# Performance work log

Measured on AMD Instinct MI355X. Metric: run time of the kernel, lower is better.

Reference implementation:

```python
import jax, jax.numpy as jnp
import numpy as np

D_MODEL = 256
D_STATE = 64
D_CONV = 4
EXPAND = 2
HEADDIM = 16
D_INNER = EXPAND * D_MODEL            # 512
NHEADS = D_INNER // HEADDIM           # 32
CONV_DIM = D_INNER + 2 * D_STATE      # 640 (ngroups=1)
D_IN_PROJ = 2 * D_INNER + 2 * D_STATE + NHEADS  # 1184
BATCH = 256
SEQ = 200


def _ln(x, g, b, eps=1e-12):
    m = jnp.mean(x, axis=-1, keepdims=True)
    v = jnp.mean((x - m) ** 2, axis=-1, keepdims=True)
    return (x - m) * jax.lax.rsqrt(v + eps) * g + b


def setup_inputs() -> dict:
    key = jax.random.key(0)
    ks = jax.random.split(key, 16)
    def gn(i, shape, s=0.02):
        return jax.random.normal(ks[i], shape, jnp.float32) * s
    return {
        "input_tensor": jax.random.normal(ks[0], (BATCH, SEQ, D_MODEL), jnp.float32),
        # Mamba2 params
        "in_proj_w": gn(1, (D_MODEL, D_IN_PROJ)),
        "conv_w": gn(2, (CONV_DIM, D_CONV), 0.1),
        "conv_b": jnp.zeros((CONV_DIM,), jnp.float32),
        "dt_bias": gn(3, (NHEADS,), 0.1),
        "A_log": jnp.log(jax.random.uniform(ks[4], (NHEADS,), jnp.float32, 1.0, 16.0)),
        "D_skip": jnp.ones((NHEADS,), jnp.float32),
        "rms_w": jnp.ones((D_INNER,), jnp.float32),
        "out_proj_w": gn(5, (D_INNER, D_MODEL)),
        # Layer norms / mixers
        "ln_g": jnp.ones((D_MODEL,), jnp.float32),
        "ln_b": jnp.zeros((D_MODEL,), jnp.float32),
        "filt_w": gn(6, (1, SEQ // 2 + 1, D_MODEL, 2), 0.02),
        "filt_ln_g": jnp.ones((D_MODEL,), jnp.float32),
        "filt_ln_b": jnp.zeros((D_MODEL,), jnp.float32),
        "alpha": jax.random.uniform(ks[7], (D_MODEL,), jnp.float32),
        "beta": jax.random.uniform(ks[8], (D_MODEL,), jnp.float32),
        # FFN
        "ffn_w1": gn(9, (D_MODEL, 4 * D_MODEL)),
        "ffn_b1": jnp.zeros((4 * D_MODEL,), jnp.float32),
        "ffn_w2": gn(10, (4 * D_MODEL, D_MODEL)),
        "ffn_b2": jnp.zeros((D_MODEL,), jnp.float32),
        "ffn_ln_g": jnp.ones((D_MODEL,), jnp.float32),
        "ffn_ln_b": jnp.zeros((D_MODEL,), jnp.float32),
    }


def _mamba2(x, in_proj_w, conv_w, conv_b, dt_bias, A_log, D_skip, rms_w, out_proj_w):
    b, l, _ = x.shape
    zxbcdt = x @ in_proj_w                                  # [b,l,1184]
    z, xBC, dt = jnp.split(zxbcdt, [D_INNER, D_INNER + CONV_DIM], axis=-1)
    # depthwise causal conv over time + SiLU
    xp = jnp.pad(xBC, ((0, 0), (D_CONV - 1, 0), (0, 0)))
    conv = conv_b + sum(conv_w[:, k] * xp[:, k:k + l, :] for k in range(D_CONV))
    xBC = jax.nn.silu(conv)
    xs, Bm, Cm = jnp.split(xBC, [D_INNER, D_INNER + D_STATE], axis=-1)
    xh = xs.reshape(b, l, NHEADS, HEADDIM)
    dt = jax.nn.softplus(dt + dt_bias)                      # [b,l,h]
    A = -jnp.exp(A_log)                                     # [h]
    dA = jnp.exp(dt * A)                                    # [b,l,h]
    dtx = dt[..., None] * xh                                # [b,l,h,p]

    def step(state, inp):
        dA_t, dtx_t, B_t, C_t = inp
        # state: [b,h,p,n]
        state = dA_t[:, :, None, None] * state + dtx_t[..., None] * B_t[:, None, None, :]
        y_t = jnp.einsum('bhpn,bn->bhp', state, C_t)
        return state, y_t

    state0 = jnp.zeros((b, NHEADS, HEADDIM, D_STATE), x.dtype)
    _, y = jax.lax.scan(step, state0,
                        (jnp.moveaxis(dA, 1, 0), jnp.moveaxis(dtx, 1, 0),
                         jnp.moveaxis(Bm, 1, 0), jnp.moveaxis(Cm, 1, 0)))
    y = jnp.moveaxis(y, 0, 1) + D_skip[None, None, :, None] * xh   # skip connection
    y = y.reshape(b, l, D_INNER)
    # gated RMSNorm: rmsnorm(y * silu(z)) * w
    g = y * jax.nn.silu(z)
    g = g * jax.lax.rsqrt(jnp.mean(g * g, axis=-1, keepdims=True) + 1e-5) * rms_w
    return g @ out_proj_w


def reference(input_tensor, in_proj_w, conv_w, conv_b, dt_bias, A_log, D_skip,
              rms_w, out_proj_w, ln_g, ln_b, filt_w, filt_ln_g, filt_ln_b,
              alpha, beta, ffn_w1, ffn_b1, ffn_w2, ffn_b2, ffn_ln_g, ffn_ln_b):
    x = input_tensor
    h1 = _mamba2(x, in_proj_w, conv_w, conv_b, dt_bias, A_log, D_skip, rms_w, out_proj_w)
    h1 = _ln(h1 + x, ln_g, ln_b)
    # FFT filter branch
    xf = jnp.fft.rfft(x, axis=1, norm='ortho')
    w = filt_w[..., 0] + 1j * filt_w[..., 1]                # [1,101,d]
    xi = jnp.fft.irfft(xf * w, n=SEQ, axis=1, norm='ortho').astype(x.dtype)
    h2 = _ln(xi + x, filt_ln_g, filt_ln_b)
    h = alpha * h1 + beta * h2
    hid = jax.nn.gelu(h @ ffn_w1 + ffn_b1, approximate=False) @ ffn_w2 + ffn_b2
    return _ln(hid + h, ffn_ln_g, ffn_ln_b)
```

## Files before the change

kernel.cpp:

```cpp
#include <hip/hip_runtime.h>
#include <math.h>

#define BATCHN 256
#define SEQ 200
#define DMODEL 256
#define DINNER 512
#define NH 32
#define HD 16
#define DSTATE 64
#define DINPROJ 1184
#define XBCLD 672
#define BL (BATCHN*SEQ)
#define NF 101
#define NJ 202
#define XBASE 655360
#define TC 20
#define NCH 10
#define XIOFF 8500000

typedef __attribute__((ext_vector_type(8))) short bf16x8;
typedef __attribute__((ext_vector_type(4))) float f32x4;

__device__ inline unsigned short f2bf(float f) {
    union { float f; unsigned u; } v; v.f = f;
    unsigned r = v.u + 0x7FFFu + ((v.u >> 16) & 1u);
    return (unsigned short)(r >> 16);
}
__device__ inline float bf2f(unsigned short h) {
    union { unsigned u; float f; } v; v.u = ((unsigned)h) << 16;
    return v.f;
}

#define GLOAD16(src, dst) __builtin_amdgcn_global_load_lds( \
    (const __attribute__((address_space(1))) void*)(src),   \
    (__attribute__((address_space(3))) void*)(dst), 16, 0, 0)

__global__ void init_dft_kernel(unsigned short* __restrict__ EF, unsigned short* __restrict__ EI)
{
    const float ang = 6.28318530717958647692f / 200.0f;
    int idx = blockIdx.x * 256 + threadIdx.x;
    if (idx < 256 * SEQ) {
        int f = idx / SEQ, t = idx - f * SEQ;
        float v;
        if (f <= 100) { int ph = (f * t) % 200; v = cosf(ang * (float)ph); }
        else if (f <= 201) { int ff = f - 101; int ph = (ff * t) % 200; v = -sinf(ang * (float)ph); }
        else v = 0.f;
        EF[idx] = f2bf(v);
    } else if (idx < 256 * SEQ + 256 * 256) {
        int j2 = idx - 256 * SEQ;
        int t = j2 >> 8, j = j2 & 255;
        float v;
        if (t >= 200) v = 0.f;
        else if (j == 0) v = 1.0f / 200.0f;
        else if (j == 100) v = ((t & 1) ? -1.0f : 1.0f) / 200.0f;
        else if (j < 100) { int ph = (j * t) % 200; v = 2.0f * cosf(ang * (float)ph) / 200.0f; }
        else if (j >= 202 || j == 101 || j == 201) v = 0.0f;
        else { int f = j - 101; int ph = (f * t) % 200; v = -2.0f * sinf(ang * (float)ph) / 200.0f; }
        EI[j2] = f2bf(v);
    }
}

__global__ void pack_wT_kernel(const float* __restrict__ src, unsigned short* __restrict__ dst,
                               int srcld, int coloff, int N, int K)
{
    int idx = blockIdx.x * 256 + threadIdx.x;
    if (idx >= N * K) return;
    int n = idx / K, k = idx - n * K;
    dst[idx] = f2bf(src[(long long)k * srcld + coloff + n]);
}

__global__ void f2bf_kernel(const float* __restrict__ X, unsigned short* __restrict__ O)
{
    long long i = ((long long)blockIdx.x * 256 + threadIdx.x) * 8;
    float4 a = ((const float4*)(X + i))[0];
    float4 b = ((const float4*)(X + i))[1];
    uint4 o;
    o.x = (unsigned)f2bf(a.x) | ((unsigned)f2bf(a.y) << 16);
    o.y = (unsigned)f2bf(a.z) | ((unsigned)f2bf(a.w) << 16);
    o.z = (unsigned)f2bf(b.x) | ((unsigned)f2bf(b.y) << 16);
    o.w = (unsigned)f2bf(b.z) | ((unsigned)f2bf(b.w) << 16);
    *(uint4*)(O + i) = o;
}

__global__ void xT_kernel(const float* __restrict__ X, unsigned short* __restrict__ XT)
{
    __shared__ float tile[32][33];
    int b = blockIdx.z, t0 = blockIdx.x * 32, d0 = blockIdx.y * 32;
    int tx = threadIdx.x & 31, ty = threadIdx.x >> 5;
    const float* xb = X + (long long)b * SEQ * DMODEL;
#pragma unroll
    for (int i = 0; i < 4; i++) {
        int t = t0 + ty + i * 8;
        tile[ty + i * 8][tx] = (t < SEQ) ? xb[(long long)t * DMODEL + d0 + tx] : 0.f;
    }
    __syncthreads();
    unsigned short* xtb = XT + (long long)b * DMODEL * SEQ;
#pragma unroll
    for (int i = 0; i < 4; i++) {
        int d = d0 + ty + i * 8;
        int t = t0 + tx;
        if (t < SEQ) xtb[(long long)d * SEQ + t] = f2bf(tile[tx][ty + i * 8]);
    }
}

template<int ACT, int CBF>
__global__ __launch_bounds__(256) void mgemm_kernel(
    const unsigned short* __restrict__ Ab, const unsigned short* __restrict__ BTp,
    void* __restrict__ Cp, const float* __restrict__ bias,
    int M, int N, int K, int lda, int ldbt, int ldc,
    long long sA, long long sBT, long long sC)
{
    __shared__ unsigned short As[128 * 32];
    __shared__ unsigned short Bs[128 * 32];
    const unsigned short* Aa = Ab + (long long)blockIdx.z * sA;
    const unsigned short* Bt = BTp + (long long)blockIdx.z * sBT;
    float* Cf = (float*)Cp + (CBF ? 0 : (long long)blockIdx.z * sC);
    unsigned short* Cb = (unsigned short*)Cp + (CBF ? (long long)blockIdx.z * sC : 0);

    int m0 = blockIdx.y * 128, n0 = blockIdx.x * 128;
    int tid = threadIdx.x;
    int srow = tid >> 1, skb = (tid & 1) * 16;
    int w = tid >> 6, l = tid & 63;
    int wr = w >> 1, wc = w & 1;
    int fr = l & 15, fk = l >> 4;
    int glr = (w << 4) + (l >> 2);
    int glc = (l & 3) << 3;
    bool fullM = (m0 + 128 <= M);
    bool fullN = (n0 + 128 <= N);

    f32x4 acc[4][4] = {};

    for (int k0 = 0; k0 < K; k0 += 32) {
        bool kedge = (k0 + 32 > K);
        if (fullM && !kedge) {
            GLOAD16(Aa + (long long)(m0 + glr) * lda + k0 + glc,      &As[w << 9]);
            GLOAD16(Aa + (long long)(m0 + 64 + glr) * lda + k0 + glc, &As[2048 + (w << 9)]);
        } else {
            int gm = m0 + srow;
            unsigned short* dst = &As[srow * 32 + skb];
#pragma unroll
            for (int i = 0; i < 16; i++) {
                int gk = k0 + skb + i;
                dst[i] = (gm < M && gk < K) ? Aa[(long long)gm * lda + gk] : (unsigned short)0;
            }
        }
        if (fullN && !kedge) {
            GLOAD16(Bt + (long long)(n0 + glr) * ldbt + k0 + glc,      &Bs[w << 9]);
            GLOAD16(Bt + (long long)(n0 + 64 + glr) * ldbt + k0 + glc, &Bs[2048 + (w << 9)]);
        } else {
            int gn = n0 + srow;
            unsigned short* dst = &Bs[srow * 32 + skb];
#pragma unroll
            for (int i = 0; i < 16; i++) {
                int gk = k0 + skb + i;
                dst[i] = (gn < N && gk < K) ? Bt[(long long)gn * ldbt + gk] : (unsigned short)0;
            }
        }
        __syncthreads();
        bf16x8 a[4], b[4];
#pragma unroll
        for (int i = 0; i < 4; i++) {
            a[i] = *(const bf16x8*)&As[(wr * 64 + i * 16 + fr) * 32 + fk * 8];
            b[i] = *(const bf16x8*)&Bs[(wc * 64 + i * 16 + fr) * 32 + fk * 8];
        }
#pragma unroll
        for (int i = 0; i < 4; i++)
#pragma unroll
            for (int j = 0; j < 4; j++)
                acc[i][j] = __builtin_amdgcn_mfma_f32_16x16x32_bf16(a[i], b[j], acc[i][j], 0, 0, 0);
        __syncthreads();
    }

#pragma unroll
    for (int i = 0; i < 4; i++) {
        int gr0 = m0 + wr * 64 + i * 16 + fk * 4;
#pragma unroll
        for (int j = 0; j < 4; j++) {
            int gc = n0 + wc * 64 + j * 16 + fr;
            if (gc >= N) continue;
            float bv = bias ? bias[gc] : 0.f;
#pragma unroll
            for (int r = 0; r < 4; r++) {
                int gr = gr0 + r;
                if (gr >= M) continue;
                float v = acc[i][j][r] + bv;
                if (ACT == 1) v = 0.5f * v * (1.f + erff(v * 0.70710678118654752f));
                long long ci = (long long)gr * ldc + gc;
                if (CBF) Cb[ci] = f2bf(v);
                else Cf[ci] = v;
            }
        }
    }
}

__global__ void convbc_kernel(const float* __restrict__ XBC, const float* __restrict__ conv_w,
                              const float* __restrict__ conv_b, const float* __restrict__ dt_bias,
                              const float* __restrict__ A_log,
                              float* __restrict__ BCb, float* __restrict__ DTb, float* __restrict__ DAb)
{
    int row = blockIdx.x;
    int b = row / SEQ, l = row - b * SEQ;
    int tid = threadIdx.x;
    if (tid < 128) {
        int ch = 512 + tid;
        float acc = conv_b[ch];
#pragma unroll
        for (int k = 0; k < 4; k++) {
            int lt = l + k - 3;
            if (lt >= 0)
                acc = fmaf(conv_w[ch * 4 + k], XBC[(long long)(b * SEQ + lt) * XBCLD + ch], acc);
        }
        BCb[(long long)row * 128 + tid] = acc * __builtin_amdgcn_rcpf(1.f + __expf(-acc));
    } else if (tid < 160) {
        int h = tid - 128;
        float draw = XBC[(long long)row * XBCLD + 640 + h] + dt_bias[h];
        float dtv = (draw > 20.f) ? draw : log1pf(__expf(draw));
        DTb[(long long)row * NH + h] = dtv;
        DAb[(long long)row * NH + h] = __expf(-__expf(A_log[h]) * dtv);
    }
}

__device__ __forceinline__ void sstep(
    float raw, float dtv, float da,
    const float4& qb0, const float4& qb1, const float4& qb2, const float4& qb3,
    const float4& qc0, const float4& qc1, const float4& qc2, const float4& qc3,
    float cw0, float cw1, float cw2, float cw3, float cb, float ds,
    float* st, float& w0, float& w1, float& w2,
    int lane, float* __restrict__ yaddr)
{
    float cvv = cb + cw0 * w0 + cw1 * w1 + cw2 * w2 + cw3 * raw;
    float xhv = cvv * __builtin_amdgcn_rcpf(1.f + __expf(-cvv));
    w0 = w1; w1 = w2; w2 = raw;
    float xv = dtv * xhv;
    float p0, p1, p2, p3;
    st[0]  = fmaf(da, st[0],  xv * qb0.x); p0 = st[0]  * qc0.x;
    st[1]  = fmaf(da, st[1],  xv * qb0.y); p1 = st[1]  * qc0.y;
    st[2]  = fmaf(da, st[2],  xv * qb0.z); p2 = st[2]  * qc0.z;
    st[3]  = fmaf(da, st[3],  xv * qb0.w); p3 = st[3]  * qc0.w;
    st[4]  = fmaf(da, st[4],  xv * qb1.x); p0 = fmaf(st[4],  qc1.x, p0);
    st[5]  = fmaf(da, st[5],  xv * qb1.y); p1 = fmaf(st[5],  qc1.y, p1);
    st[6]  = fmaf(da, st[6],  xv * qb1.z); p2 = fmaf(st[6],  qc1.z, p2);
    st[7]  = fmaf(da, st[7],  xv * qb1.w); p3 = fmaf(st[7],  qc1.w, p3);
    st[8]  = fmaf(da, st[8],  xv * qb2.x); p0 = fmaf(st[8],  qc2.x, p0);
    st[9]  = fmaf(da, st[9],  xv * qb2.y); p1 = fmaf(st[9],  qc2.y, p1);
    st[10] = fmaf(da, st[10], xv * qb2.z); p2 = fmaf(st[10], qc2.z, p2);
    st[11] = fmaf(da, st[11], xv * qb2.w); p3 = fmaf(st[11], qc2.w, p3);
    st[12] = fmaf(da, st[12], xv * qb3.x); p0 = fmaf(st[12], qc3.x, p0);
    st[13] = fmaf(da, st[13], xv * qb3.y); p1 = fmaf(st[13], qc3.y, p1);
    st[14] = fmaf(da, st[14], xv * qb3.z); p2 = fmaf(st[14], qc3.z, p2);
    st[15] = fmaf(da, st[15], xv * qb3.w); p3 = fmaf(st[15], qc3.w, p3);
    float part = (p0 + p1) + (p2 + p3);
    part += __shfl_xor(part, 16);
    part += __shfl_xor(part, 32);
    if (lane < HD) *yaddr = part + ds * xhv;
}

__global__ __launch_bounds__(256) void scan7_kernel(
    const float* __restrict__ DTb, const float* __restrict__ DAb,
    float* __restrict__ XBC, const float* __restrict__ BCb,
    const float* __restrict__ Dsk,
    const float* __restrict__ conv_w, const float* __restrict__ conv_b)
{
    __shared__ float sbc[2][TC][128];
    __shared__ unsigned short sx[2][TC][128];
    __shared__ float sdt[2][TC][8];
    __shared__ float sda[2][TC][8];
    int tid = threadIdx.x;
    int wv = tid >> 6, lane = tid & 63;
    int bid = blockIdx.x;
    int b = bid >> 2, hq = (bid & 3) * 8;
    long long rowb = (long long)b * SEQ;

    for (int i = tid; i < TC * 32; i += 256) {
        int r = i >> 5, c = i & 31;
        ((float4*)&sbc[0][r][0])[c] = ((const float4*)(BCb + (rowb + r) * 128))[c];
    }
    for (int i = tid; i < TC * 64; i += 256) {
        int r = i >> 6, c2 = i & 63;
        float2 v = *(const float2*)(XBC + (rowb + r) * XBCLD + hq * 16 + (c2 << 1));
        *(unsigned*)&sx[0][r][c2 << 1] = (unsigned)f2bf(v.x) | ((unsigned)f2bf(v.y) << 16);
    }
    for (int i = tid; i < TC * 8; i += 256) {
        int t = i >> 3, j = i & 7;
        sdt[0][t][j] = DTb[(rowb + t) * NH + hq + j];
        sda[0][t][j] = DAb[(rowb + t) * NH + hq + j];
    }
    __syncthreads();

    int p = lane & 15, g = lane >> 4;
    int hA = hq + wv, hB = hq + 4 + wv;
    int chA = hA * HD + p, chB = hB * HD + p;
    float cwA0 = conv_w[chA * 4 + 0], cwA1 = conv_w[chA * 4 + 1];
    float cwA2 = conv_w[chA * 4 + 2], cwA3 = conv_w[chA * 4 + 3];
    float cbA = conv_b[chA];
    float cwB0 = conv_w[chB * 4 + 0], cwB1 = conv_w[chB * 4 + 1];
    float cwB2 = conv_w[chB * 4 + 2], cwB3 = conv_w[chB * 4 + 3];
    float cbB = conv_b[chB];
    float dsA = Dsk[hA], dsB = Dsk[hB];
    int xcA = wv * 16 + p, xcB = (4 + wv) * 16 + p;
    float* ypA = XBC + rowb * XBCLD + hA * HD + p;
    float* ypB = XBC + rowb * XBCLD + hB * HD + p;
    float stA[16], stB[16];
#pragma unroll
    for (int r = 0; r < 16; r++) { stA[r] = 0.f; stB[r] = 0.f; }
    float wA0 = 0.f, wA1 = 0.f, wA2 = 0.f;
    float wB0 = 0.f, wB1 = 0.f, wB2 = 0.f;

    for (int c = 0; c < NCH; c++) {
        int cur = c & 1;
        if (c + 1 < NCH) {
            int nb = cur ^ 1;
            long long tb = rowb + (c + 1) * TC;
            for (int i = tid; i < TC * 32; i += 256) {
                int r = i >> 5, cc = i & 31;
                ((float4*)&sbc[nb][r][0])[cc] = ((const float4*)(BCb + (tb + r) * 128))[cc];
            }
            for (int i = tid; i < TC * 64; i += 256) {
                int r = i >> 6, c2 = i & 63;
                float2 v = *(const float2*)(XBC + (tb + r) * XBCLD + hq * 16 + (c2 << 1));
                *(unsigned*)&sx[nb][r][c2 << 1] = (unsigned)f2bf(v.x) | ((unsigned)f2bf(v.y) << 16);
            }
            for (int i = tid; i < TC * 8; i += 256) {
                int t = i >> 3, j = i & 7;
                sdt[nb][t][j] = DTb[(tb + t) * NH + hq + j];
                sda[nb][t][j] = DAb[(tb + t) * NH + hq + j];
            }
        }
        int tbase = c * TC;
        for (int t = 0; t < TC; t++) {
            int gt = tbase + t;
            const float4* qb = (const float4*)&sbc[cur][t][g * 16];
            const float4* qc = (const float4*)&sbc[cur][t][64 + g * 16];
            float4 qb0 = qb[0], qb1 = qb[1], qb2 = qb[2], qb3 = qb[3];
            float4 qc0 = qc[0], qc1 = qc[1], qc2 = qc[2], qc3 = qc[3];
            float rawA = bf2f(sx[cur][t][xcA]);
            float rawB = bf2f(sx[cur][t][xcB]);
            sstep(rawA, sdt[cur][t][wv], sda[cur][t][wv], qb0, qb1, qb2, qb3, qc0, qc1, qc2, qc3,
                  cwA0, cwA1, cwA2, cwA3, cbA, dsA, stA, wA0, wA1, wA2,
                  lane, ypA + (long long)gt * XBCLD);
            sstep(rawB, sdt[cur][t][4 + wv], sda[cur][t][4 + wv], qb0, qb1, qb2, qb3, qc0, qc1, qc2, qc3,
                  cwB0, cwB1, cwB2, cwB3, cbB, dsB, stB, wB0, wB1, wB2,
                  lane, ypB + (long long)gt * XBCLD);
        }
        __syncthreads();
    }
}

__global__ __launch_bounds__(256) void gate_kernel(
    float* __restrict__ XBC, const unsigned short* __restrict__ Zbf,
    const float* __restrict__ rms_w)
{
    int row = blockIdx.x * 4 + (threadIdx.x >> 6);
    int lane = threadIdx.x & 63;
    float* yrow = XBC + (long long)row * XBCLD + lane * 8;
    const unsigned short* zrow = Zbf + (long long)row * 512 + lane * 8;
    float4 y0 = ((const float4*)yrow)[0];
    float4 y1 = ((const float4*)yrow)[1];
    uint4 zq = ((const uint4*)zrow)[0];
    float yv[8] = { y0.x, y0.y, y0.z, y0.w, y1.x, y1.y, y1.z, y1.w };
    float zv[8];
    zv[0] = bf2f((unsigned short)(zq.x & 0xFFFF)); zv[1] = bf2f((unsigned short)(zq.x >> 16));
    zv[2] = bf2f((unsigned short)(zq.y & 0xFFFF)); zv[3] = bf2f((unsigned short)(zq.y >> 16));
    zv[4] = bf2f((unsigned short)(zq.z & 0xFFFF)); zv[5] = bf2f((unsigned short)(zq.z >> 16));
    zv[6] = bf2f((unsigned short)(zq.w & 0xFFFF)); zv[7] = bf2f((unsigned short)(zq.w >> 16));
    float a[8]; float ss = 0.f;
#pragma unroll
    for (int i = 0; i < 8; i++) {
        float z = zv[i];
        a[i] = yv[i] * (z * __builtin_amdgcn_rcpf(1.f + __expf(-z)));
        ss = fmaf(a[i], a[i], ss);
    }
#pragma unroll
    for (int m = 1; m < 64; m <<= 1) ss += __shfl_xor(ss, m);
    float sc = rsqrtf(ss * (1.f / 512.f) + 1e-5f);
    const float* rw = rms_w + lane * 8;
    float4 r0 = ((const float4*)rw)[0];
    float4 r1 = ((const float4*)rw)[1];
    float rv[8] = { r0.x, r0.y, r0.z, r0.w, r1.x, r1.y, r1.z, r1.w };
    uint4 o;
    o.x = (unsigned)f2bf(a[0] * sc * rv[0]) | ((unsigned)f2bf(a[1] * sc * rv[1]) << 16);
    o.y = (unsigned)f2bf(a[2] * sc * rv[2]) | ((unsigned)f2bf(a[3] * sc * rv[3]) << 16);
    o.z = (unsigned)f2bf(a[4] * sc * rv[4]) | ((unsigned)f2bf(a[5] * sc * rv[5]) << 16);
    o.w = (unsigned)f2bf(a[6] * sc * rv[6]) | ((unsigned)f2bf(a[7] * sc * rv[7]) << 16);
    unsigned short* grow = (unsigned short*)(XBC + (long long)row * XBCLD);
    ((uint4*)grow)[lane] = o;
}

__global__ void lnadd_bf_kernel(const unsigned short* __restrict__ A, const float* __restrict__ Bb,
                                const float* __restrict__ g, const float* __restrict__ be,
                                float* __restrict__ O)
{
    int row = blockIdx.x * 4 + (threadIdx.x >> 6);
    int lane = threadIdx.x & 63;
    long long base = (long long)row * DMODEL + lane * 4;
    float v[4]; float s1 = 0.f;
#pragma unroll
    for (int i = 0; i < 4; i++) { float a = bf2f(A[base + i]) + Bb[base + i]; v[i] = a; s1 += a; }
#pragma unroll
    for (int m = 1; m < 64; m <<= 1) s1 += __shfl_xor(s1, m);
    float mean = s1 * (1.f / 256.f);
    float s2 = 0.f;
#pragma unroll
    for (int i = 0; i < 4; i++) { float d = v[i] - mean; s2 = fmaf(d, d, s2); }
#pragma unroll
    for (int m = 1; m < 64; m <<= 1) s2 += __shfl_xor(s2, m);
    float r = rsqrtf(s2 * (1.f / 256.f) + 1e-12f);
#pragma unroll
    for (int i = 0; i < 4; i++)
        O[base + i] = (v[i] - mean) * r * g[lane * 4 + i] + be[lane * 4 + i];
}

__global__ void combine2_kernel(const float* __restrict__ XI, const float* __restrict__ X,
                                float* __restrict__ MO, unsigned short* __restrict__ HB,
                                const float* __restrict__ lg, const float* __restrict__ lb,
                                const float* __restrict__ fg, const float* __restrict__ fb,
                                const float* __restrict__ al, const float* __restrict__ bt)
{
    int row = blockIdx.x * 4 + (threadIdx.x >> 6);
    int lane = threadIdx.x & 63;
    long long base = (long long)row * DMODEL + lane * 4;
    int bb = row / SEQ, ll = row - bb * SEQ;
    long long xib = (long long)bb * 65536 + ll * 256 + lane * 4;
    float u[4], v[4]; float su = 0.f, sv = 0.f;
#pragma unroll
    for (int i = 0; i < 4; i++) {
        float xv = X[base + i];
        float a = MO[base + i] + xv;
        float b = XI[xib + i] + xv;
        u[i] = a; v[i] = b; su += a; sv += b;
    }
#pragma unroll
    for (int m = 1; m < 64; m <<= 1) { su += __shfl_xor(su, m); sv += __shfl_xor(sv, m); }
    float mu = su * (1.f / 256.f), mv = sv * (1.f / 256.f);
    float qu = 0.f, qv = 0.f;
#pragma unroll
    for (int i = 0; i < 4; i++) {
        float du = u[i] - mu; qu = fmaf(du, du, qu);
        float dv = v[i] - mv; qv = fmaf(dv, dv, qv);
    }
#pragma unroll
    for (int m = 1; m < 64; m <<= 1) { qu += __shfl_xor(qu, m); qv += __shfl_xor(qv, m); }
    float ru = rsqrtf(qu * (1.f / 256.f) + 1e-12f);
    float rv = rsqrtf(qv * (1.f / 256.f) + 1e-12f);
#pragma unroll
    for (int i = 0; i < 4; i++) {
        int d = lane * 4 + i;
        float h1 = (u[i] - mu) * ru * lg[d] + lb[d];
        float h2 = (v[i] - mv) * rv * fg[d] + fb[d];
        float h = al[d] * h1 + bt[d] * h2;
        MO[base + i] = h;
        HB[base + i] = f2bf(h);
    }
}

__global__ void filt_kernel(unsigned short* __restrict__ XF, const float* __restrict__ W)
{
    long long idx = (long long)blockIdx.x * 256 + threadIdx.x;
    if (idx >= (long long)BATCHN * DMODEL * NF) return;
    int f = (int)(idx % NF);
    int d = (int)((idx / NF) % DMODEL);
    int b = (int)(idx / ((long long)NF * DMODEL));
    long long base = ((long long)b * DMODEL + d) * 256;
    float re = bf2f(XF[base + f]);
    float im = bf2f(XF[base + 101 + f]);
    float wr = W[((long long)f * DMODEL + d) * 2];
    float wi = W[((long long)f * DMODEL + d) * 2 + 1];
    XF[base + f]       = f2bf(re * wr - im * wi);
    XF[base + 101 + f] = f2bf(re * wi + im * wr);
}

extern "C" void kernel_launch(void* const* d_in, const int* in_sizes, int n_in,
                              void* d_out, int out_size, void* d_ws, size_t ws_size,
                              hipStream_t stream)
{
    const float* x          = (const float*)d_in[0];
    const float* in_proj_w  = (const float*)d_in[1];
    const float* conv_w     = (const float*)d_in[2];
    const float* conv_b     = (const float*)d_in[3];
    const float* dt_bias    = (const float*)d_in[4];
    const float* A_log      = (const float*)d_in[5];
    const float* D_skip     = (const float*)d_in[6];
    const float* rms_w      = (const float*)d_in[7];
    const float* out_proj_w = (const float*)d_in[8];
    const float* ln_g       = (const float*)d_in[9];
    const float* ln_b       = (const float*)d_in[10];
    const float* filt_w     = (const float*)d_in[11];
    const float* filt_ln_g  = (const float*)d_in[12];
    const float* filt_ln_b  = (const float*)d_in[13];
    const float* alpha      = (const float*)d_in[14];
    const float* beta       = (const float*)d_in[15];
    const float* ffn_w1     = (const float*)d_in[16];
    const float* ffn_b1     = (const float*)d_in[17];
    const float* ffn_w2     = (const float*)d_in[18];
    const float* ffn_b2     = (const float*)d_in[19];
    const float* ffn_ln_g   = (const float*)d_in[20];
    const float* ffn_ln_b   = (const float*)d_in[21];
    float* out = (float*)d_out;
    float* ws = (float*)d_ws;

    unsigned short* WP   = (unsigned short*)(ws + 81920);
    unsigned short* ipwT = WP;
    unsigned short* opwT = ipwT + 672 * 256;
    unsigned short* w1T  = opwT + 256 * 512;
    unsigned short* w2T  = w1T + 1024 * 256;
    unsigned short* zwT  = w2T + 256 * 1024;
    unsigned short* EFbf = zwT + 512 * 256;
    unsigned short* EIbf = EFbf + 256 * SEQ;
    float* XBC = ws + XBASE;
    float* BCb = XBC + (long long)BL * XBCLD;
    float* DTb = BCb + (long long)BL * 128;
    float* DAb = DTb + (long long)BL * NH;
    float* MO  = DAb + (long long)BL * NH;
    unsigned short* Zbf = (unsigned short*)MO;
    unsigned short* xbf  = (unsigned short*)BCb;
    unsigned short* xTbf = (unsigned short*)BCb;
    unsigned short* MObf = (unsigned short*)BCb;
    unsigned short* Gbf = (unsigned short*)XBC;
    unsigned short* XFT = (unsigned short*)XBC;
    float* XI  = XBC + XIOFF;
    unsigned short* HID = (unsigned short*)XBC;
    unsigned short* FFO = (unsigned short*)(XBC + 26500000);

    init_dft_kernel<<<dim3((256 * SEQ + 256 * 256 + 255) / 256), dim3(256), 0, stream>>>(EFbf, EIbf);
    pack_wT_kernel<<<dim3((672 * 256 + 255) / 256), dim3(256), 0, stream>>>(in_proj_w, ipwT, DINPROJ, 512, 672, 256);
    pack_wT_kernel<<<dim3((512 * 256 + 255) / 256), dim3(256), 0, stream>>>(in_proj_w, zwT, DINPROJ, 0, 512, 256);
    pack_wT_kernel<<<dim3((256 * 512 + 255) / 256), dim3(256), 0, stream>>>(out_proj_w, opwT, 256, 0, 256, 512);
    pack_wT_kernel<<<dim3((1024 * 256 + 255) / 256), dim3(256), 0, stream>>>(ffn_w1, w1T, 1024, 0, 1024, 256);
    pack_wT_kernel<<<dim3((256 * 1024 + 255) / 256), dim3(256), 0, stream>>>(ffn_w2, w2T, 256, 0, 256, 1024);
    f2bf_kernel<<<dim3(BL * DMODEL / 2048), dim3(256), 0, stream>>>(x, xbf);

    mgemm_kernel<0,0><<<dim3(6, BL / 128, 1), dim3(256), 0, stream>>>(
        xbf, ipwT, XBC, nullptr, BL, 672, 256, 256, 256, 672, 0, 0, 0);

    mgemm_kernel<0,1><<<dim3(4, BL / 128, 1), dim3(256), 0, stream>>>(
        xbf, zwT, Zbf, nullptr, BL, 512, 256, 256, 256, 512, 0, 0, 0);

    convbc_kernel<<<dim3(BL), dim3(192), 0, stream>>>(XBC, conv_w, conv_b, dt_bias, A_log,
                                                      BCb, DTb, DAb);

    scan7_kernel<<<dim3(BATCHN * 4), dim3(256), 0, stream>>>(DTb, DAb, XBC, BCb, D_skip,
                                                             conv_w, conv_b);

    xT_kernel<<<dim3(7, 8, BATCHN), dim3(256), 0, stream>>>(x, xTbf);

    gate_kernel<<<dim3(BL / 4), dim3(256), 0, stream>>>(XBC, Zbf, rms_w);

    mgemm_kernel<0,0><<<dim3(2, BL / 128, 1), dim3(256), 0, stream>>>(
        Gbf, opwT, MO, nullptr, BL, 256, 512, 1344, 512, 256, 0, 0, 0);

    mgemm_kernel<0,1><<<dim3(2, 2, BATCHN), dim3(256), 0, stream>>>(
        xTbf, EFbf, XFT, nullptr, 256, 256, SEQ, SEQ, SEQ, 256,
        (long long)DMODEL * SEQ, 0, 65536);

    filt_kernel<<<dim3((BATCHN * DMODEL * NF + 255) / 256), dim3(256), 0, stream>>>(XFT, filt_w);

    mgemm_kernel<0,0><<<dim3(2, 2, BATCHN), dim3(256), 0, stream>>>(
        EIbf, XFT, XI, nullptr, 256, 256, 256, 256, 256, 256,
        0, 65536, 65536);

    combine2_kernel<<<dim3(BL / 4), dim3(256), 0, stream>>>(XI, x, MO, MObf,
                                                            ln_g, ln_b, filt_ln_g, filt_ln_b,
                                                            alpha, beta);

    mgemm_kernel<1,1><<<dim3(8, BL / 128, 1), dim3(256), 0, stream>>>(
        MObf, w1T, HID, ffn_b1, BL, 1024, 256, 256, 256, 1024, 0, 0, 0);

    mgemm_kernel<0,1><<<dim3(2, BL / 128, 1), dim3(256), 0, stream>>>(
        HID, w2T, FFO, ffn_b2, BL, 256, 1024, 1024, 1024, 256, 0, 0, 0);

    lnadd_bf_kernel<<<dim3(BL / 4), dim3(256), 0, stream>>>(FFO, MO, ffn_ln_g, ffn_ln_b, out);
}
```

Baseline: 859.9 us.

## Fuse setup packing, merge in-projection GEMMs, decouple scan output from state update

Six weight-packing and bf16-conversion launches become one setup kernel. The two in-projection GEMMs (z and xBC/dt) become a single GEMM over all 1184 columns whose epilogue routes outputs to separate buffers. The scan step now computes y from the previous state, using a precomputed per-row B·C dot product from convbc (y = da*C·h_prev + xv*(B·C) + D*x), so the readout no longer waits on the state update. This trims launch overhead and a second pass over the activations, and shortens the scan dependency chain, at the cost of a partial last N tile and an extra reduction in convbc.

```diff
diff --git a/kernel.cpp b/kernel.cpp
--- a/kernel.cpp
+++ b/kernel.cpp
@@ -12,7 +12,6 @@
 #define XBCLD 672
 #define BL (BATCHN*SEQ)
 #define NF 101
-#define NJ 202
 #define XBASE 655360
 #define TC 20
 #define NCH 10
@@ -60,26 +59,42 @@
     }
 }
 
-__global__ void pack_wT_kernel(const float* __restrict__ src, unsigned short* __restrict__ dst,
-                               int srcld, int coloff, int N, int K)
-{
-    int idx = blockIdx.x * 256 + threadIdx.x;
-    if (idx >= N * K) return;
-    int n = idx / K, k = idx - n * K;
-    dst[idx] = f2bf(src[(long long)k * srcld + coloff + n]);
-}
-
-__global__ void f2bf_kernel(const float* __restrict__ X, unsigned short* __restrict__ O)
-{
-    long long i = ((long long)blockIdx.x * 256 + threadIdx.x) * 8;
-    float4 a = ((const float4*)(X + i))[0];
-    float4 b = ((const float4*)(X + i))[1];
-    uint4 o;
-    o.x = (unsigned)f2bf(a.x) | ((unsigned)f2bf(a.y) << 16);
-    o.y = (unsigned)f2bf(a.z) | ((unsigned)f2bf(a.w) << 16);
-    o.z = (unsigned)f2bf(b.x) | ((unsigned)f2bf(b.y) << 16);
-    o.w = (unsigned)f2bf(b.z) | ((unsigned)f2bf(b.w) << 16);
-    *(uint4*)(O + i) = o;
+#define S0 303104
+#define S1 131072
+#define S2 262144
+#define S3 262144
+#define S4 1638400
+__global__ void setup_kernel(const float* __restrict__ ipw, const float* __restrict__ opw,
+                             const float* __restrict__ w1, const float* __restrict__ w2,
+                             const float* __restrict__ X,
+                             unsigned short* __restrict__ wTall, unsigned short* __restrict__ opwT,
+                             unsigned short* __restrict__ w1T, unsigned short* __restrict__ w2T,
+                             unsigned short* __restrict__ xbf)
+{
+    long long idx = (long long)blockIdx.x * 256 + threadIdx.x;
+    if (idx < S0) { int n = (int)(idx / 256), k = (int)(idx % 256);
+        wTall[idx] = f2bf(ipw[(long long)k * DINPROJ + n]); return; }
+    idx -= S0;
+    if (idx < S1) { int n = (int)(idx / 512), k = (int)(idx % 512);
+        opwT[idx] = f2bf(opw[(long long)k * 256 + n]); return; }
+    idx -= S1;
+    if (idx < S2) { int n = (int)(idx / 256), k = (int)(idx % 256);
+        w1T[idx] = f2bf(w1[(long long)k * 1024 + n]); return; }
+    idx -= S2;
+    if (idx < S3) { int n = (int)(idx / 1024), k = (int)(idx % 1024);
+        w2T[idx] = f2bf(w2[(long long)k * 256 + n]); return; }
+    idx -= S3;
+    if (idx < S4) {
+        long long i = idx * 8;
+        float4 a = ((const float4*)(X + i))[0];
+        float4 b = ((const float4*)(X + i))[1];
+        uint4 o;
+        o.x = (unsigned)f2bf(a.x) | ((unsigned)f2bf(a.y) << 16);
+        o.y = (unsigned)f2bf(a.z) | ((unsigned)f2bf(a.w) << 16);
+        o.z = (unsigned)f2bf(b.x) | ((unsigned)f2bf(b.y) << 16);
+        o.w = (unsigned)f2bf(b.z) | ((unsigned)f2bf(b.w) << 16);
+        *(uint4*)(xbf + i) = o;
+    }
 }
 
 __global__ void xT_kernel(const float* __restrict__ X, unsigned short* __restrict__ XT)
@@ -193,14 +208,82 @@
     }
 }
 
+__global__ __launch_bounds__(256) void mgemm_proj(
+    const unsigned short* __restrict__ Aa, const unsigned short* __restrict__ Bt,
+    float* __restrict__ XBCout, unsigned short* __restrict__ Zout)
+{
+    __shared__ unsigned short As[128 * 32];
+    __shared__ unsigned short Bs[128 * 32];
+    const int N = DINPROJ;
+    int m0 = blockIdx.y * 128, n0 = blockIdx.x * 128;
+    int tid = threadIdx.x;
+    int srow = tid >> 1, skb = (tid & 1) * 16;
+    int w = tid >> 6, l = tid & 63;
+    int wr = w >> 1, wc = w & 1;
+    int fr = l & 15, fk = l >> 4;
+    int glr = (w << 4) + (l >> 2);
+    int glc = (l & 3) << 3;
+    bool fullN = (n0 + 128 <= N);
+
+    f32x4 acc[4][4] = {};
+
+    for (int k0 = 0; k0 < 256; k0 += 32) {
+        GLOAD16(Aa + (long long)(m0 + glr) * 256 + k0 + glc,      &As[w << 9]);
+        GLOAD16(Aa + (long long)(m0 + 64 + glr) * 256 + k0 + glc, &As[2048 + (w << 9)]);
+        if (fullN) {
+            GLOAD16(Bt + (long long)(n0 + glr) * 256 + k0 + glc,      &Bs[w << 9]);
+            GLOAD16(Bt + (long long)(n0 + 64 + glr) * 256 + k0 + glc, &Bs[2048 + (w << 9)]);
+        } else {
+            int gn = n0 + srow;
+            unsigned short* dst = &Bs[srow * 32 + skb];
+#pragma unroll
+            for (int i = 0; i < 16; i++)
+                dst[i] = (gn < N) ? Bt[(long long)gn * 256 + k0 + skb + i] : (unsigned short)0;
+        }
+        __syncthreads();
+        bf16x8 a[4], b[4];
+#pragma unroll
+        for (int i = 0; i < 4; i++) {
+            a[i] = *(const bf16x8*)&As[(wr * 64 + i * 16 + fr) * 32 + fk * 8];
+            b[i] = *(const bf16x8*)&Bs[(wc * 64 + i * 16 + fr) * 32 + fk * 8];
+        }
+#pragma unroll
+        for (int i = 0; i < 4; i++)
+#pragma unroll
+            for (int j = 0; j < 4; j++)
+                acc[i][j] = __builtin_amdgcn_mfma_f32_16x16x32_bf16(a[i], b[j], acc[i][j], 0, 0, 0);
+        __syncthreads();
+    }
+
+#pragma unroll
+    for (int i = 0; i < 4; i++) {
+        int gr0 = m0 + wr * 64 + i * 16 + fk * 4;
+#pragma unroll
+        for (int j = 0; j < 4; j++) {
+            int gc = n0 + wc * 64 + j * 16 + fr;
+            if (gc >= N) continue;
+#pragma unroll
+            for (int r = 0; r < 4; r++) {
+                int gr = gr0 + r;
+                float v = acc[i][j][r];
+                if (gc < 512) Zout[(long long)gr * 512 + gc] = f2bf(v);
+                else XBCout[(long long)gr * XBCLD + (gc - 512)] = v;
+            }
+        }
+    }
+}
+
 __global__ void convbc_kernel(const float* __restrict__ XBC, const float* __restrict__ conv_w,
                               const float* __restrict__ conv_b, const float* __restrict__ dt_bias,
                               const float* __restrict__ A_log,
-                              float* __restrict__ BCb, float* __restrict__ DTb, float* __restrict__ DAb)
-{
+                              float* __restrict__ BCb, float* __restrict__ DTb, float* __restrict__ DAb,
+                              float* __restrict__ BCF)
+{
+    __shared__ float sB[64];
     int row = blockIdx.x;
     int b = row / SEQ, l = row - b * SEQ;
     int tid = threadIdx.x;
+    float v = 0.f;
     if (tid < 128) {
         int ch = 512 + tid;
         float acc = conv_b[ch];
@@ -210,7 +293,9 @@
             if (lt >= 0)
                 acc = fmaf(conv_w[ch * 4 + k], XBC[(long long)(b * SEQ + lt) * XBCLD + ch], acc);
         }
-        BCb[(long long)row * 128 + tid] = acc * __builtin_amdgcn_rcpf(1.f + __expf(-acc));
+        v = acc * __builtin_amdgcn_rcpf(1.f + __expf(-acc));
+        BCb[(long long)row * 128 + tid] = v;
+        if (tid < 64) sB[tid] = v;
     } else if (tid < 160) {
         int h = tid - 128;
         float draw = XBC[(long long)row * XBCLD + 640 + h] + dt_bias[h];
@@ -218,10 +303,18 @@
         DTb[(long long)row * NH + h] = dtv;
         DAb[(long long)row * NH + h] = __expf(-__expf(A_log[h]) * dtv);
     }
-}
-
-__device__ __forceinline__ void sstep(
-    float raw, float dtv, float da,
+    __syncthreads();
+    if (tid >= 64 && tid < 128) {
+        int n = tid - 64;
+        float prod = sB[n] * v;
+#pragma unroll
+        for (int m = 1; m < 64; m <<= 1) prod += __shfl_xor(prod, m);
+        if (n == 0) BCF[row] = prod;
+    }
+}
+
+__device__ __forceinline__ void sstep2(
+    float raw, float dtv, float da, float bc,
     const float4& qb0, const float4& qb1, const float4& qb2, const float4& qb3,
     const float4& qc0, const float4& qc1, const float4& qc2, const float4& qc3,
     float cw0, float cw1, float cw2, float cw3, float cb, float ds,
@@ -232,39 +325,56 @@
     float xhv = cvv * __builtin_amdgcn_rcpf(1.f + __expf(-cvv));
     w0 = w1; w1 = w2; w2 = raw;
     float xv = dtv * xhv;
-    float p0, p1, p2, p3;
-    st[0]  = fmaf(da, st[0],  xv * qb0.x); p0 = st[0]  * qc0.x;
-    st[1]  = fmaf(da, st[1],  xv * qb0.y); p1 = st[1]  * qc0.y;
-    st[2]  = fmaf(da, st[2],  xv * qb0.z); p2 = st[2]  * qc0.z;
-    st[3]  = fmaf(da, st[3],  xv * qb0.w); p3 = st[3]  * qc0.w;
-    st[4]  = fmaf(da, st[4],  xv * qb1.x); p0 = fmaf(st[4],  qc1.x, p0);
-    st[5]  = fmaf(da, st[5],  xv * qb1.y); p1 = fmaf(st[5],  qc1.y, p1);
-    st[6]  = fmaf(da, st[6],  xv * qb1.z); p2 = fmaf(st[6],  qc1.z, p2);
-    st[7]  = fmaf(da, st[7],  xv * qb1.w); p3 = fmaf(st[7],  qc1.w, p3);
-    st[8]  = fmaf(da, st[8],  xv * qb2.x); p0 = fmaf(st[8],  qc2.x, p0);
-    st[9]  = fmaf(da, st[9],  xv * qb2.y); p1 = fmaf(st[9],  qc2.y, p1);
-    st[10] = fmaf(da, st[10], xv * qb2.z); p2 = fmaf(st[10], qc2.z, p2);
-    st[11] = fmaf(da, st[11], xv * qb2.w); p3 = fmaf(st[11], qc2.w, p3);
-    st[12] = fmaf(da, st[12], xv * qb3.x); p0 = fmaf(st[12], qc3.x, p0);
-    st[13] = fmaf(da, st[13], xv * qb3.y); p1 = fmaf(st[13], qc3.y, p1);
-    st[14] = fmaf(da, st[14], xv * qb3.z); p2 = fmaf(st[14], qc3.z, p2);
-    st[15] = fmaf(da, st[15], xv * qb3.w); p3 = fmaf(st[15], qc3.w, p3);
+    float p0 = st[0]  * qc0.x;
+    float p1 = st[1]  * qc0.y;
+    float p2 = st[2]  * qc0.z;
+    float p3 = st[3]  * qc0.w;
+    p0 = fmaf(st[4],  qc1.x, p0);
+    p1 = fmaf(st[5],  qc1.y, p1);
+    p2 = fmaf(st[6],  qc1.z, p2);
+    p3 = fmaf(st[7],  qc1.w, p3);
+    p0 = fmaf(st[8],  qc2.x, p0);
+    p1 = fmaf(st[9],  qc2.y, p1);
+    p2 = fmaf(st[10], qc2.z, p2);
+    p3 = fmaf(st[11], qc2.w, p3);
+    p0 = fmaf(st[12], qc3.x, p0);
+    p1 = fmaf(st[13], qc3.y, p1);
+    p2 = fmaf(st[14], qc3.z, p2);
+    p3 = fmaf(st[15], qc3.w, p3);
+    st[0]  = fmaf(da, st[0],  xv * qb0.x);
+    st[1]  = fmaf(da, st[1],  xv * qb0.y);
+    st[2]  = fmaf(da, st[2],  xv * qb0.z);
+    st[3]  = fmaf(da, st[3],  xv * qb0.w);
+    st[4]  = fmaf(da, st[4],  xv * qb1.x);
+    st[5]  = fmaf(da, st[5],  xv * qb1.y);
+    st[6]  = fmaf(da, st[6],  xv * qb1.z);
+    st[7]  = fmaf(da, st[7],  xv * qb1.w);
+    st[8]  = fmaf(da, st[8],  xv * qb2.x);
+    st[9]  = fmaf(da, st[9],  xv * qb2.y);
+    st[10] = fmaf(da, st[10], xv * qb2.z);
+    st[11] = fmaf(da, st[11], xv * qb2.w);
+    st[12] = fmaf(da, st[12], xv * qb3.x);
+    st[13] = fmaf(da, st[13], xv * qb3.y);
+    st[14] = fmaf(da, st[14], xv * qb3.z);
+    st[15] = fmaf(da, st[15], xv * qb3.w);
     float part = (p0 + p1) + (p2 + p3);
     part += __shfl_xor(part, 16);
     part += __shfl_xor(part, 32);
-    if (lane < HD) *yaddr = part + ds * xhv;
-}
-
-__global__ __launch_bounds__(256) void scan7_kernel(
+    if (lane < HD) *yaddr = fmaf(da, part, fmaf(xv, bc, ds * xhv));
+}
+
+__global__ __launch_bounds__(256) void scan7b_kernel(
     const float* __restrict__ DTb, const float* __restrict__ DAb,
     float* __restrict__ XBC, const float* __restrict__ BCb,
     const float* __restrict__ Dsk,
-    const float* __restrict__ conv_w, const float* __restrict__ conv_b)
+    const float* __restrict__ conv_w, const float* __restrict__ conv_b,
+    const float* __restrict__ BCF)
 {
     __shared__ float sbc[2][TC][128];
     __shared__ unsigned short sx[2][TC][128];
     __shared__ float sdt[2][TC][8];
     __shared__ float sda[2][TC][8];
+    __shared__ float sbcf[2][TC];
     int tid = threadIdx.x;
     int wv = tid >> 6, lane = tid & 63;
     int bid = blockIdx.x;
@@ -285,6 +395,7 @@
         sdt[0][t][j] = DTb[(rowb + t) * NH + hq + j];
         sda[0][t][j] = DAb[(rowb + t) * NH + hq + j];
     }
+    if (tid < TC) sbcf[0][tid] = BCF[rowb + tid];
     __syncthreads();
 
     int p = lane & 15, g = lane >> 4;
@@ -325,6 +436,7 @@
                 sdt[nb][t][j] = DTb[(tb + t) * NH + hq + j];
                 sda[nb][t][j] = DAb[(tb + t) * NH + hq + j];
             }
+            if (tid < TC) sbcf[nb][tid] = BCF[tb + tid];
         }
         int tbase = c * TC;
         for (int t = 0; t < TC; t++) {
@@ -335,12 +447,15 @@
             float4 qc0 = qc[0], qc1 = qc[1], qc2 = qc[2], qc3 = qc[3];
             float rawA = bf2f(sx[cur][t][xcA]);
             float rawB = bf2f(sx[cur][t][xcB]);
-            sstep(rawA, sdt[cur][t][wv], sda[cur][t][wv], qb0, qb1, qb2, qb3, qc0, qc1, qc2, qc3,
-                  cwA0, cwA1, cwA2, cwA3, cbA, dsA, stA, wA0, wA1, wA2,
-                  lane, ypA + (long long)gt * XBCLD);
-            sstep(rawB, sdt[cur][t][4 + wv], sda[cur][t][4 + wv], qb0, qb1, qb2, qb3, qc0, qc1, qc2, qc3,
-                  cwB0, cwB1, cwB2, cwB3, cbB, dsB, stB, wB0, wB1, wB2,
-                  lane, ypB + (long long)gt * XBCLD);
+            float bc = sbcf[cur][t];
+            sstep2(rawA, sdt[cur][t][wv], sda[cur][t][wv], bc,
+                   qb0, qb1, qb2, qb3, qc0, qc1, qc2, qc3,
+                   cwA0, cwA1, cwA2, cwA3, cbA, dsA, stA, wA0, wA1, wA2,
+                   lane, ypA + (long long)gt * XBCLD);
+            sstep2(rawB, sdt[cur][t][4 + wv], sda[cur][t][4 + wv], bc,
+                   qb0, qb1, qb2, qb3, qc0, qc1, qc2, qc3,
+                   cwB0, cwB1, cwB2, cwB3, cbB, dsB, stB, wB0, wB1, wB2,
+                   lane, ypB + (long long)gt * XBCLD);
         }
         __syncthreads();
     }
@@ -498,19 +613,19 @@
     float* out = (float*)d_out;
     float* ws = (float*)d_ws;
 
-    unsigned short* WP   = (unsigned short*)(ws + 81920);
-    unsigned short* ipwT = WP;
-    unsigned short* opwT = ipwT + 672 * 256;
-    unsigned short* w1T  = opwT + 256 * 512;
-    unsigned short* w2T  = w1T + 1024 * 256;
-    unsigned short* zwT  = w2T + 256 * 1024;
-    unsigned short* EFbf = zwT + 512 * 256;
-    unsigned short* EIbf = EFbf + 256 * SEQ;
+    unsigned short* WP    = (unsigned short*)(ws + 81920);
+    unsigned short* wTall = WP;
+    unsigned short* opwT  = wTall + 1184 * 256;
+    unsigned short* w1T   = opwT + 256 * 512;
+    unsigned short* w2T   = w1T + 1024 * 256;
+    unsigned short* EFbf  = w2T + 256 * 1024;
+    unsigned short* EIbf  = EFbf + 256 * SEQ;
     float* XBC = ws + XBASE;
     float* BCb = XBC + (long long)BL * XBCLD;
     float* DTb = BCb + (long long)BL * 128;
     float* DAb = DTb + (long long)BL * NH;
     float* MO  = DAb + (long long)BL * NH;
+    float* BCF = MO + (long long)BL * DMODEL;
     unsigned short* Zbf = (unsigned short*)MO;
     unsigned short* xbf  = (unsigned short*)BCb;
     unsigned short* xTbf = (unsigned short*)BCb;
@@ -522,24 +637,16 @@
     unsigned short* FFO = (unsigned short*)(XBC + 26500000);
 
     init_dft_kernel<<<dim3((256 * SEQ + 256 * 256 + 255) / 256), dim3(256), 0, stream>>>(EFbf, EIbf);
-    pack_wT_kernel<<<dim3((672 * 256 + 255) / 256), dim3(256), 0, stream>>>(in_proj_w, ipwT, DINPROJ, 512, 672, 256);
-    pack_wT_kernel<<<dim3((512 * 256 + 255) / 256), dim3(256), 0, stream>>>(in_proj_w, zwT, DINPROJ, 0, 512, 256);
-    pack_wT_kernel<<<dim3((256 * 512 + 255) / 256), dim3(256), 0, stream>>>(out_proj_w, opwT, 256, 0, 256, 512);
-    pack_wT_kernel<<<dim3((1024 * 256 + 255) / 256), dim3(256), 0, stream>>>(ffn_w1, w1T, 1024, 0, 1024, 256);
-    pack_wT_kernel<<<dim3((256 * 1024 + 255) / 256), dim3(256), 0, stream>>>(ffn_w2, w2T, 256, 0, 256, 1024);
-    f2bf_kernel<<<dim3(BL * DMODEL / 2048), dim3(256), 0, stream>>>(x, xbf);
-
-    mgemm_kernel<0,0><<<dim3(6, BL / 128, 1), dim3(256), 0, stream>>>(
-        xbf, ipwT, XBC, nullptr, BL, 672, 256, 256, 256, 672, 0, 0, 0);
-
-    mgemm_kernel<0,1><<<dim3(4, BL / 128, 1), dim3(256), 0, stream>>>(
-        xbf, zwT, Zbf, nullptr, BL, 512, 256, 256, 256, 512, 0, 0, 0);
+    setup_kernel<<<dim3((S0 + S1 + S2 + S3 + S4) / 256), dim3(256), 0, stream>>>(
+        in_proj_w, out_proj_w, ffn_w1, ffn_w2, x, wTall, opwT, w1T, w2T, xbf);
+
+    mgemm_proj<<<dim3(10, BL / 128), dim3(256), 0, stream>>>(xbf, wTall, XBC, Zbf);
 
     convbc_kernel<<<dim3(BL), dim3(192), 0, stream>>>(XBC, conv_w, conv_b, dt_bias, A_log,
-                                                      BCb, DTb, DAb);
-
-    scan7_kernel<<<dim3(BATCHN * 4), dim3(256), 0, stream>>>(DTb, DAb, XBC, BCb, D_skip,
-                                                             conv_w, conv_b);
+                                                      BCb, DTb, DAb, BCF);
+
+    scan7b_kernel<<<dim3(BATCHN * 4), dim3(256), 0, stream>>>(DTb, DAb, XBC, BCb, D_skip,
+                                                              conv_w, conv_b, BCF);
 
     xT_kernel<<<dim3(7, 8, BATCHN), dim3(256), 0, stream>>>(x, xTbf);
 
```

Measured after the change: 814.2 us. 5.3% less time.
